# Optimization experiments

Measured on AMD Instinct MI355X. Metric: run time of the kernel, lower is better.

The kernel has to match this reference:

```python
import jax, jax.numpy as jnp
import numpy as np
from math import sqrt

# Dims: B batch, L frames, N points/frame, DIM transformer dim,
# J joints, M memory slots per joint, FD final_dim = DIM//8, OUT = 3*J
B, L, N, DIM = 4, 24, 512, 1024
J, M, FD, OUT = 24, 64, 128, 72


def setup_inputs() -> dict:
    key = jax.random.key(0)
    ks = jax.random.split(key, 8)
    w = lambda k, shape: jax.random.normal(k, shape, jnp.float32) * 0.02
    return {
        "feat": jax.random.normal(ks[0], (B, L, N, DIM), jnp.float32),
        "seg_w": w(ks[1], (J, DIM)),
        "seg_b": jnp.zeros((J,), jnp.float32),
        "pc_w": w(ks[2], (FD, DIM)),
        "pc_b": jnp.zeros((FD,), jnp.float32),
        "mem": jax.random.normal(ks[3], (FD, J * M), jnp.float32),
        "ln_g": jnp.ones((FD,), jnp.float32),
        "ln_b": jnp.zeros((FD,), jnp.float32),
        "w1": w(ks[4], (FD // 2, FD)),
        "b1": jnp.zeros((FD // 2,), jnp.float32),
        "w2": w(ks[5], (OUT, FD // 2)),
        "b2": jnp.zeros((OUT,), jnp.float32),
    }


def forward_mem(y, s, mem):
    # y: (B, Nt, D) point features; s: (B, Nt, J) seg weights; mem: (D, J*M)
    Bn, Nt, D = y.shape
    # affinity of every token to every (joint, slot) memory entry
    logits = jnp.einsum('dk,bnd->bkn', mem, y) / sqrt(D)            # (B, J*M, Nt)
    # per-joint segmentation weighting of the logits
    logits = logits.reshape(Bn, J, M, Nt) * s.transpose(0, 2, 1)[:, :, None, :]
    attn = jax.nn.softmax(logits.reshape(Bn, J * M, Nt), axis=1)     # over memory slots
    return jnp.einsum('dk,bkn->bnd', mem, attn)                      # (B, Nt, D)


def reference(feat, seg_w, seg_b, pc_w, pc_b, mem, ln_g, ln_b, w1, b1, w2, b2):
    Bn, Lf, Np, C = feat.shape
    # seg_head: 1x1 conv == per-point linear -> softmax over joints
    seg = jnp.einsum('blnc,jc->blnj', feat, seg_w) + seg_b           # (B,L,N,J)
    seg = jax.nn.softmax(seg.reshape(Bn, Lf * Np, J), axis=-1)       # (B, L*N, J)
    seg_out = seg.reshape(Bn, Lf, Np, J).transpose(0, 1, 3, 2)       # (B,L,J,N)
    # pc_head: per-point projection to final_dim
    pc = (jnp.einsum('blnc,fc->blnf', feat, pc_w) + pc_b).reshape(Bn, Lf * Np, FD)
    rec = forward_mem(pc, seg, mem)                                  # (B, L*N, FD)
    loss_rec = jnp.mean((rec - pc) ** 2)
    skl = jnp.max(rec, axis=1)                                       # (B, FD)
    # skl_head: LayerNorm -> Linear -> GELU -> Linear
    mu = jnp.mean(skl, axis=-1, keepdims=True)
    var = jnp.var(skl, axis=-1, keepdims=True)
    h = (skl - mu) * jax.lax.rsqrt(var + 1e-5) * ln_g + ln_b
    h = jax.nn.gelu(h @ w1.T + b1, approximate=False)
    skl_out = h @ w2.T + b2                                          # (B, OUT)
    return skl_out, seg_out, loss_rec
```

## Files before the change

kernel.cpp:

```cpp
#include <hip/hip_runtime.h>

typedef __bf16 bf16_t;
typedef bf16_t bf16x8 __attribute__((ext_vector_type(8)));
typedef float f32x4 __attribute__((ext_vector_type(4)));
typedef unsigned short u16;

#define MFMA16 __builtin_amdgcn_mfma_f32_16x16x32_bf16

#define NT_TOK   12288
#define T_TOK    49152

#define WS_PC    0
#define WS_S     25165824
#define WS_WP    29884416
#define WS_MTP   30212096
#define WS_MFP   30605312
#define WS_SKL   30998528
#define WS_LOSS  31000576

__device__ __forceinline__ u16 f2bf(float f) {
  union { bf16_t h; u16 u; } c; c.h = (bf16_t)f; return c.u;
}

__device__ __forceinline__ void atomic_max_f32(float* a, float v) {
  if (v >= 0.f) atomicMax((int*)a, __float_as_int(v));
  else atomicMin((unsigned int*)a, (unsigned int)__float_as_int(v));
}

__global__ void k_init(const float* __restrict__ seg_w, const float* __restrict__ pc_w,
                       const float* __restrict__ mem,
                       u16* __restrict__ Wp, u16* __restrict__ mTp, u16* __restrict__ mFp,
                       float* __restrict__ skl, float* __restrict__ loss)
{
  int i = blockIdx.x * 256 + threadIdx.x;
  union { u16 s[8]; uint4 v; } u;
  if (i < 20480) {
    int lane = i & 63, blk = i >> 6;
    int kc = blk / 10, t = blk - kc * 10;
    int n = lane & 15, q = lane >> 4;
    int row = t * 16 + n;
    int k0 = kc * 32 + q * 8;
    #pragma unroll
    for (int e = 0; e < 8; ++e) {
      float v = 0.f;
      if (row < 24) v = seg_w[row * 1024 + k0 + e];
      else if (row < 152) v = pc_w[(row - 24) * 1024 + k0 + e];
      u.s[e] = f2bf(v);
    }
    *(uint4*)(Wp + (size_t)i * 8) = u.v;
  } else if ((i -= 20480) < 24576) {
    int lane = i & 63, blk = i >> 6;
    int j = blk >> 4, rem = blk & 15, wv = rem >> 2, ks = rem & 3;
    int n = lane & 15, q = lane >> 4;
    int slot = j * 64 + wv * 16 + n;
    int d0 = ks * 32 + q * 8;
    #pragma unroll
    for (int e = 0; e < 8; ++e)
      u.s[e] = f2bf(mem[(size_t)(d0 + e) * 1536 + slot]);
    *(uint4*)(mTp + (size_t)i * 8) = u.v;
  } else if ((i -= 24576) < 24576) {
    int lane = i & 63, blk = i >> 6;
    int j = blk >> 4, h = (blk >> 3) & 1, wv = (blk >> 1) & 3, ft = blk & 1;
    int n = lane & 15, q = lane >> 4;
    int f = wv * 32 + ft * 16 + n;
    int s0 = j * 64 + h * 32 + q * 8;
    #pragma unroll
    for (int e = 0; e < 8; ++e)
      u.s[e] = f2bf(mem[(size_t)f * 1536 + s0 + e]);
    *(uint4*)(mFp + (size_t)i * 8) = u.v;
  } else if ((i -= 24576) < 512) {
    skl[i] = -__builtin_inff();
  } else if (i == 512) {
    *loss = 0.f;
  }
}

__global__ __launch_bounds__(256, 3) void k_proj(
    const float* __restrict__ feat, const u16* __restrict__ Wp,
    const float* __restrict__ seg_b, const float* __restrict__ pc_b,
    float* __restrict__ pc_out, float* __restrict__ s_out, float* __restrict__ out_seg)
{
  const int tid = threadIdx.x;
  const int w = tid >> 6;
  const int lane = tid & 63;
  const int n = lane & 15;
  const int q = lane >> 4;
  const int base = blockIdx.x * 64;

  f32x4 acc[10];
  #pragma unroll
  for (int t = 0; t < 10; ++t) acc[t] = (f32x4){0.f, 0.f, 0.f, 0.f};

  const float* fp0 = feat + (size_t)(base + w * 16 + n) * 1024 + q * 8;
  const u16* wfrag = Wp + (size_t)lane * 8;

  float4 fb[4][2];
  #pragma unroll
  for (int p = 0; p < 4; ++p) {
    const float4* a = (const float4*)(fp0 + p * 32);
    fb[p][0] = a[0];
    fb[p][1] = a[1];
  }

  for (int kb = 0; kb < 8; ++kb) {
    #pragma unroll
    for (int p = 0; p < 4; ++p) {
      const int kc = kb * 4 + p;
      float4 x0 = fb[p][0], y0 = fb[p][1];
      bf16x8 bw[10];
      #pragma unroll
      for (int t = 0; t < 10; ++t)
        bw[t] = *(const bf16x8*)(wfrag + (size_t)(kc * 10 + t) * 512);
      if (kb < 7) {
        const float4* a = (const float4*)(fp0 + (kc + 4) * 32);
        fb[p][0] = a[0];
        fb[p][1] = a[1];
      }
      bf16x8 af;
      af[0] = (bf16_t)x0.x; af[1] = (bf16_t)x0.y; af[2] = (bf16_t)x0.z; af[3] = (bf16_t)x0.w;
      af[4] = (bf16_t)y0.x; af[5] = (bf16_t)y0.y; af[6] = (bf16_t)y0.z; af[7] = (bf16_t)y0.w;
      #pragma unroll
      for (int t = 0; t < 10; ++t)
        acc[t] = MFMA16(af, bw[t], acc[t], 0, 0, 0);
    }
  }

  #pragma unroll
  for (int r = 0; r < 4; ++r) {
    const int token = base + w * 16 + q * 4 + r;
    float v0 = acc[0][r] + seg_b[n];
    float v1 = (n < 8) ? (acc[1][r] + seg_b[16 + n]) : -__builtin_inff();
    float mx = fmaxf(v0, v1);
    #pragma unroll
    for (int d2 = 1; d2 < 16; d2 <<= 1) mx = fmaxf(mx, __shfl_xor(mx, d2, 16));
    float e0 = __expf(v0 - mx);
    float e1 = (n < 8) ? __expf(v1 - mx) : 0.f;
    float sm = e0 + e1;
    #pragma unroll
    for (int d2 = 1; d2 < 16; d2 <<= 1) sm += __shfl_xor(sm, d2, 16);
    float is = 1.f / sm;
    float s0v = e0 * is, s1v = e1 * is;
    s_out[(size_t)token * 24 + n] = s0v;
    if (n < 8) s_out[(size_t)token * 24 + 16 + n] = s1v;
    const int b = token / NT_TOK;
    const int rem = token - b * NT_TOK;
    const int l = rem >> 9, p = rem & 511;
    float* so = out_seg + ((size_t)(b * 24 + l) * 24) * 512 + p;
    so[(size_t)n * 512] = s0v;
    if (n < 8) so[(size_t)(16 + n) * 512] = s1v;
    #pragma unroll
    for (int t = 1; t < 10; ++t) {
      int col = t * 16 + n;
      if (col >= 24 && col < 152) {
        pc_out[(size_t)token * 128 + (col - 24)] = acc[t][r] + pc_b[col - 24];
      }
    }
  }
}

#define AS_S     0
#define AS_P     6656
#define AS_LW    15872
#define AS_RL    16896
#define AS_TOT   16912

__global__ __launch_bounds__(256, 3) void k_attn(
    const float* __restrict__ pc, const float* __restrict__ s_in,
    const u16* __restrict__ mFp, const u16* __restrict__ mTp,
    float* __restrict__ skl, float* __restrict__ loss)
{
  __shared__ __align__(16) char smem[AS_TOT];
  float* s_tile = (float*)(smem + AS_S);
  u16* Pl  = (u16*)(smem + AS_P);
  float* lw  = (float*)(smem + AS_LW);
  float* redL = (float*)(smem + AS_RL);

  const int tid = threadIdx.x;
  const int w = tid >> 6, lane = tid & 63, n = lane & 15, q = lane >> 4;
  const int base = blockIdx.x * 64;

  for (int i = tid; i < 1536; i += 256) {
    int t = i / 24, jj = i - t * 24;
    s_tile[t * 26 + jj] = s_in[(size_t)base * 24 + i];
  }

  bf16x8 qf[4][4];
  #pragma unroll
  for (int tt = 0; tt < 4; ++tt)
    #pragma unroll
    for (int ks = 0; ks < 4; ++ks) {
      const float4* qp = (const float4*)(pc + (size_t)(base + tt * 16 + n) * 128 + ks * 32 + q * 8);
      float4 x = qp[0], y = qp[1];
      bf16x8 a;
      a[0] = (bf16_t)x.x; a[1] = (bf16_t)x.y; a[2] = (bf16_t)x.z; a[3] = (bf16_t)x.w;
      a[4] = (bf16_t)y.x; a[5] = (bf16_t)y.y; a[6] = (bf16_t)y.z; a[7] = (bf16_t)y.w;
      qf[tt][ks] = a;
    }

  f32x4 o[4][2];
  #pragma unroll
  for (int tt = 0; tt < 4; ++tt) {
    o[tt][0] = (f32x4){0.f, 0.f, 0.f, 0.f};
    o[tt][1] = (f32x4){0.f, 0.f, 0.f, 0.f};
  }
  float l_acc[4] = {0.f, 0.f, 0.f, 0.f};

  const u16* mT_frag = mTp + (size_t)(w * 4) * 512 + lane * 8;
  const u16* mF_frag = mFp + (size_t)(w * 2) * 512 + lane * 8;

  const float invs = 0.088388347648318447f;
  __syncthreads();

  for (int j = 0; j < 24; ++j) {
    f32x4 sacc[4];
    #pragma unroll
    for (int tt = 0; tt < 4; ++tt) sacc[tt] = (f32x4){0.f, 0.f, 0.f, 0.f};
    #pragma unroll
    for (int ks = 0; ks < 4; ++ks) {
      bf16x8 am = *(const bf16x8*)(mT_frag + (size_t)(j * 16 + ks) * 512);
      #pragma unroll
      for (int tt = 0; tt < 4; ++tt)
        sacc[tt] = MFMA16(am, qf[tt][ks], sacc[tt], 0, 0, 0);
    }

    __syncthreads();
    #pragma unroll
    for (int tt = 0; tt < 4; ++tt) {
      float sj = s_tile[(tt * 16 + n) * 26 + j] * invs;
      float p0 = __expf(sacc[tt][0] * sj);
      float p1 = __expf(sacc[tt][1] * sj);
      float p2 = __expf(sacc[tt][2] * sj);
      float p3 = __expf(sacc[tt][3] * sj);
      l_acc[tt] += (p0 + p1) + (p2 + p3);
      ushort4 pk;
      pk.x = f2bf(p0); pk.y = f2bf(p1); pk.z = f2bf(p2); pk.w = f2bf(p3);
      *(ushort4*)(&Pl[(tt * 16 + n) * 72 + w * 16 + q * 4]) = pk;
    }
    __syncthreads();

    #pragma unroll
    for (int h = 0; h < 2; ++h) {
      bf16x8 bm[2];
      #pragma unroll
      for (int ft = 0; ft < 2; ++ft)
        bm[ft] = *(const bf16x8*)(mF_frag + (size_t)(j * 16 + h * 8 + ft) * 512);
      #pragma unroll
      for (int tt = 0; tt < 4; ++tt) {
        bf16x8 pa = *(const bf16x8*)(&Pl[(tt * 16 + n) * 72 + h * 32 + q * 8]);
        o[tt][0] = MFMA16(pa, bm[0], o[tt][0], 0, 0, 0);
        o[tt][1] = MFMA16(pa, bm[1], o[tt][1], 0, 0, 0);
      }
    }
  }

  #pragma unroll
  for (int tt = 0; tt < 4; ++tt) {
    float v = l_acc[tt];
    v += __shfl_xor(v, 16, 64);
    v += __shfl_xor(v, 32, 64);
    if (q == 0) lw[w * 64 + tt * 16 + n] = v;
  }
  __syncthreads();

  float lsum = 0.f;
  float fmax2[2] = {-__builtin_inff(), -__builtin_inff()};
  #pragma unroll
  for (int tt = 0; tt < 4; ++tt) {
    f32x4 linv;
    #pragma unroll
    for (int r = 0; r < 4; ++r) {
      int tok = tt * 16 + q * 4 + r;
      float lt = lw[tok] + lw[64 + tok] + lw[128 + tok] + lw[192 + tok];
      linv[r] = 1.f / lt;
    }
    #pragma unroll
    for (int ft = 0; ft < 2; ++ft)
      #pragma unroll
      for (int r = 0; r < 4; ++r) {
        const int token = base + tt * 16 + q * 4 + r;
        const int f = w * 32 + ft * 16 + n;
        float rec = o[tt][ft][r] * linv[r];
        float d = rec - pc[(size_t)token * 128 + f];
        lsum += d * d;
        fmax2[ft] = fmaxf(fmax2[ft], rec);
      }
  }
  #pragma unroll
  for (int ft = 0; ft < 2; ++ft) {
    float v = fmax2[ft];
    v = fmaxf(v, __shfl_xor(v, 16, 64));
    v = fmaxf(v, __shfl_xor(v, 32, 64));
    if (q == 0) atomic_max_f32(&skl[(base / NT_TOK) * 128 + w * 32 + ft * 16 + n], v);
  }
  #pragma unroll
  for (int d2 = 1; d2 < 64; d2 <<= 1) lsum += __shfl_xor(lsum, d2, 64);
  if (lane == 0) redL[w] = lsum;
  __syncthreads();
  if (tid == 0) atomicAdd(loss, redL[0] + redL[1] + redL[2] + redL[3]);
}

__global__ void k_head(const float* __restrict__ skl,
                       const float* __restrict__ ln_g, const float* __restrict__ ln_b,
                       const float* __restrict__ w1, const float* __restrict__ b1,
                       const float* __restrict__ w2, const float* __restrict__ b2,
                       const float* __restrict__ loss, float* __restrict__ out)
{
  __shared__ float hbuf[128];
  __shared__ float gbuf[64];
  __shared__ float red[4];
  const int t = threadIdx.x;
  const int ln = t & 63, wv = t >> 6;
  for (int b = 0; b < 4; ++b) {
    float x = skl[b * 128 + t];
    float s1 = x, s2 = x * x;
    #pragma unroll
    for (int d = 1; d < 64; d <<= 1) {
      s1 += __shfl_xor(s1, d, 64);
      s2 += __shfl_xor(s2, d, 64);
    }
    if (ln == 0) { red[wv * 2] = s1; red[wv * 2 + 1] = s2; }
    __syncthreads();
    float mu = (red[0] + red[2]) * (1.f / 128.f);
    float var = (red[1] + red[3]) * (1.f / 128.f) - mu * mu;
    float hn = (x - mu) * rsqrtf(var + 1e-5f) * ln_g[t] + ln_b[t];
    hbuf[t] = hn;
    __syncthreads();
    if (t < 64) {
      float a = b1[t];
      for (int c = 0; c < 128; ++c) a += hbuf[c] * w1[t * 128 + c];
      gbuf[t] = 0.5f * a * (1.f + erff(a * 0.70710678118654752f));
    }
    __syncthreads();
    if (t < 72) {
      float a = b2[t];
      for (int c = 0; c < 64; ++c) a += gbuf[c] * w2[t * 64 + c];
      out[b * 72 + t] = a;
    }
    __syncthreads();
  }
  if (t == 0) out[1179936] = loss[0] * (1.f / 6291456.f);
}

extern "C" void kernel_launch(void* const* d_in, const int* in_sizes, int n_in,
                              void* d_out, int out_size, void* d_ws, size_t ws_size,
                              hipStream_t stream) {
  (void)in_sizes; (void)n_in; (void)out_size; (void)ws_size;
  const float* feat  = (const float*)d_in[0];
  const float* seg_w = (const float*)d_in[1];
  const float* seg_b = (const float*)d_in[2];
  const float* pc_w  = (const float*)d_in[3];
  const float* pc_b  = (const float*)d_in[4];
  const float* mem   = (const float*)d_in[5];
  const float* ln_g  = (const float*)d_in[6];
  const float* ln_b  = (const float*)d_in[7];
  const float* w1    = (const float*)d_in[8];
  const float* b1    = (const float*)d_in[9];
  const float* w2    = (const float*)d_in[10];
  const float* b2    = (const float*)d_in[11];

  char* ws = (char*)d_ws;
  float* pc_buf = (float*)(ws + WS_PC);
  float* s_buf  = (float*)(ws + WS_S);
  u16*   Wp     = (u16*)(ws + WS_WP);
  u16*   mTp    = (u16*)(ws + WS_MTP);
  u16*   mFp    = (u16*)(ws + WS_MFP);
  float* sklb   = (float*)(ws + WS_SKL);
  float* lossb  = (float*)(ws + WS_LOSS);
  float* out    = (float*)d_out;

  k_init<<<275, 256, 0, stream>>>(seg_w, pc_w, mem, Wp, mTp, mFp, sklb, lossb);
  k_proj<<<768, 256, 0, stream>>>(feat, Wp, seg_b, pc_b, pc_buf, s_buf, out + 288);
  k_attn<<<768, 256, 0, stream>>>(pc_buf, s_buf, mFp, mTp, sklb, lossb);
  k_head<<<1, 128, 0, stream>>>(sklb, ln_g, ln_b, w1, b1, w2, b2, lossb, out);
}
```

Baseline: 418.3 us.

## Stage projection weights through double-buffered LDS with async global-to-LDS loads

In k_proj, each wave used to read its own weight fragments straight from global memory. Now the block cooperatively loads 20KB weight chunks into a double-buffered LDS array using global_load_lds, and the feat loads are prefetched one chunk ahead. The goal is to stop the four waves from fetching the same weights redundantly and to overlap weight fetches with MFMA work. In exchange it uses 40KB of LDS per block, which may limit occupancy under launch_bounds(256,3), and adds a __syncthreads per chunk. The feat prefetch depth also drops from four k-chunks to two.

```diff
diff --git a/kernel.cpp b/kernel.cpp
--- a/kernel.cpp
+++ b/kernel.cpp
@@ -26,6 +26,10 @@
   if (v >= 0.f) atomicMax((int*)a, __float_as_int(v));
   else atomicMin((unsigned int*)a, (unsigned int)__float_as_int(v));
 }
+
+#define GLD16(g, l) __builtin_amdgcn_global_load_lds( \
+    (const __attribute__((address_space(1))) void*)(g), \
+    (__attribute__((address_space(3))) void*)(l), 16, 0, 0)
 
 __global__ void k_init(const float* __restrict__ seg_w, const float* __restrict__ pc_w,
                        const float* __restrict__ mem,
@@ -80,6 +84,8 @@
     const float* __restrict__ seg_b, const float* __restrict__ pc_b,
     float* __restrict__ pc_out, float* __restrict__ s_out, float* __restrict__ out_seg)
 {
+  __shared__ __align__(16) u16 wbuf[2][10240];
+
   const int tid = threadIdx.x;
   const int w = tid >> 6;
   const int lane = tid & 63;
@@ -92,36 +98,64 @@
   for (int t = 0; t < 10; ++t) acc[t] = (f32x4){0.f, 0.f, 0.f, 0.f};
 
   const float* fp0 = feat + (size_t)(base + w * 16 + n) * 1024 + q * 8;
-  const u16* wfrag = Wp + (size_t)lane * 8;
-
-  float4 fb[4][2];
-  #pragma unroll
-  for (int p = 0; p < 4; ++p) {
-    const float4* a = (const float4*)(fp0 + p * 32);
-    fb[p][0] = a[0];
-    fb[p][1] = a[1];
-  }
-
-  for (int kb = 0; kb < 8; ++kb) {
-    #pragma unroll
-    for (int p = 0; p < 4; ++p) {
-      const int kc = kb * 4 + p;
-      float4 x0 = fb[p][0], y0 = fb[p][1];
+
+  {
+    const u16* gW = Wp;
+    #pragma unroll
+    for (int i = 0; i < 5; ++i) {
+      const int off = i * 2048 + w * 512;
+      GLD16(gW + off + lane * 8, &wbuf[0][off]);
+    }
+  }
+  float4 fcur[2][2], fnext[2][2];
+  #pragma unroll
+  for (int kc2 = 0; kc2 < 2; ++kc2) {
+    const float4* a = (const float4*)(fp0 + kc2 * 32);
+    fcur[kc2][0] = a[0];
+    fcur[kc2][1] = a[1];
+  }
+  __syncthreads();
+
+  for (int c = 0; c < 16; ++c) {
+    const u16* lb = &wbuf[c & 1][0];
+
+    if (c < 15) {
+      const u16* gW = Wp + (size_t)(c + 1) * 10240;
+      u16* nb = &wbuf[(c + 1) & 1][0];
+      #pragma unroll
+      for (int i = 0; i < 5; ++i) {
+        const int off = i * 2048 + w * 512;
+        GLD16(gW + off + lane * 8, nb + off);
+      }
+      #pragma unroll
+      for (int kc2 = 0; kc2 < 2; ++kc2) {
+        const float4* a = (const float4*)(fp0 + ((c + 1) * 2 + kc2) * 32);
+        fnext[kc2][0] = a[0];
+        fnext[kc2][1] = a[1];
+      }
+    }
+
+    #pragma unroll
+    for (int kc2 = 0; kc2 < 2; ++kc2) {
       bf16x8 bw[10];
       #pragma unroll
       for (int t = 0; t < 10; ++t)
-        bw[t] = *(const bf16x8*)(wfrag + (size_t)(kc * 10 + t) * 512);
-      if (kb < 7) {
-        const float4* a = (const float4*)(fp0 + (kc + 4) * 32);
-        fb[p][0] = a[0];
-        fb[p][1] = a[1];
-      }
+        bw[t] = *(const bf16x8*)(lb + (size_t)(kc2 * 10 + t) * 512 + lane * 8);
+      float4 x0 = fcur[kc2][0], y0 = fcur[kc2][1];
       bf16x8 af;
       af[0] = (bf16_t)x0.x; af[1] = (bf16_t)x0.y; af[2] = (bf16_t)x0.z; af[3] = (bf16_t)x0.w;
       af[4] = (bf16_t)y0.x; af[5] = (bf16_t)y0.y; af[6] = (bf16_t)y0.z; af[7] = (bf16_t)y0.w;
       #pragma unroll
       for (int t = 0; t < 10; ++t)
         acc[t] = MFMA16(af, bw[t], acc[t], 0, 0, 0);
+    }
+
+    __syncthreads();
+
+    #pragma unroll
+    for (int kc2 = 0; kc2 < 2; ++kc2) {
+      fcur[kc2][0] = fnext[kc2][0];
+      fcur[kc2][1] = fnext[kc2][1];
     }
   }
 
```

Result: faster. 397.6 us (-5.0%).
